# Kernel optimization log

Measured on AMD Instinct MI355X. Metric: run time of the kernel, lower is better.

## Reference

```python
import jax, jax.numpy as jnp
import numpy as np

EMBED = 2048
HEADS = 32
HEAD_DIM = 64
MLP_DIM = 8192
TILE = 16
TOP_K = 12
THETA = 500000.0
EPS = 1e-5
NEG = -1e30


def setup_inputs() -> dict:
    key = jax.random.key(0)
    ks = jax.random.split(key, 9)
    B, S = 2, 1024
    w = lambda k, i, o: jax.random.normal(k, (i, o), jnp.float32) * (i ** -0.5)
    return {
        "x": jax.random.normal(ks[0], (B, S, EMBED), jnp.float32),
        "attn_norm_scale": jnp.ones((EMBED,), jnp.float32),
        "wq": w(ks[1], EMBED, HEADS * HEAD_DIM),
        "wk": w(ks[2], EMBED, HEADS * HEAD_DIM),
        "wv": w(ks[3], EMBED, HEADS * HEAD_DIM),
        "wo": w(ks[4], HEADS * HEAD_DIM, EMBED),
        "ffn_norm_scale": jnp.ones((EMBED,), jnp.float32),
        "w_gate": w(ks[5], EMBED, MLP_DIM),
        "w_up": w(ks[6], EMBED, MLP_DIM),
        "w_down": w(ks[7], MLP_DIM, EMBED),
    }


def _rmsnorm(h, g):
    return h * jax.lax.rsqrt(jnp.mean(h * h, axis=-1, keepdims=True) + EPS) * g


def _rope(t, cos, sin):
    # t: [B,S,H,D]; rotate interleaved pairs (llama precompute_freqs_cis style)
    t1, t2 = t[..., 0::2], t[..., 1::2]
    return jnp.stack([t1 * cos - t2 * sin, t1 * sin + t2 * cos], axis=-1).reshape(t.shape)


def reference(x, attn_norm_scale, wq, wk, wv, wo, ffn_norm_scale, w_gate, w_up, w_down):
    B, S, E = x.shape
    n = _rmsnorm(x, attn_norm_scale)
    q = (n @ wq).reshape(B, S, HEADS, HEAD_DIM)
    k = (n @ wk).reshape(B, S, HEADS, HEAD_DIM)
    v = (n @ wv).reshape(B, S, HEADS, HEAD_DIM)

    inv = 1.0 / (THETA ** (jnp.arange(0, HEAD_DIM, 2, dtype=jnp.float32) / HEAD_DIM))
    ang = jnp.arange(S, dtype=jnp.float32)[:, None] * inv  # [S, D/2]
    cos = jnp.cos(ang)[None, :, None, :]
    sin = jnp.sin(ang)[None, :, None, :]
    q = _rope(q, cos, sin)
    k = _rope(k, cos, sin)

    scale = HEAD_DIM ** -0.5
    scores = jnp.einsum("bqhd,bkhd->bhqk", q, k) * scale  # [B,H,S,S]
    causal = jnp.tril(jnp.ones((S, S), dtype=bool))

    # Kascade anchor: per-query top-k key-tile selection on causally-masked scores
    T = S // TILE
    masked = jnp.where(causal, scores, NEG)
    tile_logits = masked.reshape(B, HEADS, S, T, TILE).max(axis=-1)  # [B,H,S,T]
    _, idx = jax.lax.top_k(tile_logits, TOP_K)  # [B,H,S,K]
    sel = jax.nn.one_hot(idx, T, dtype=jnp.float32).sum(axis=-2) > 0  # [B,H,S,T]
    own = jax.nn.one_hot(jnp.arange(S) // TILE, T, dtype=jnp.float32)[None, None] > 0
    key_mask = jnp.repeat(sel | own, TILE, axis=-1)  # [B,H,S,S]
    allowed = key_mask & causal

    probs = jax.nn.softmax(jnp.where(allowed, scores, NEG), axis=-1)
    attn = jnp.einsum("bhqk,bkhd->bqhd", probs, v).reshape(B, S, HEADS * HEAD_DIM)
    x = x + attn @ wo

    n2 = _rmsnorm(x, ffn_norm_scale)
    mlp = (jax.nn.silu(n2 @ w_gate) * (n2 @ w_up)) @ w_down
    return x + mlp
```

## Files before the change

kernel.cpp:

```cpp
#include <hip/hip_runtime.h>
#include <math.h>

typedef __bf16 bf16_t;
typedef bf16_t bf16x8 __attribute__((ext_vector_type(8)));
typedef bf16_t bf16x2 __attribute__((ext_vector_type(2)));
typedef float f32x4 __attribute__((ext_vector_type(4)));

#define EMBED 2048
#define NHEADS 32
#define HDIM 64
#define MLP 8192
#define SEQ 1024
#define NTOK 2048
#define QKV_N 6144

__device__ __forceinline__ void async_copy16(void* lds, const void* g) {
    __builtin_amdgcn_global_load_lds(
        (const __attribute__((address_space(1))) unsigned int*)g,
        (__attribute__((address_space(3))) unsigned int*)lds, 16, 0, 0);
}

template<int CTRL>
__device__ __forceinline__ float dpp_f(float x) {
    return __int_as_float(__builtin_amdgcn_update_dpp(
        __float_as_int(x), __float_as_int(x), CTRL, 0xF, 0xF, false));
}
__device__ __forceinline__ float rowmax16(float v) {
    v = fmaxf(v, dpp_f<0x121>(v));
    v = fmaxf(v, dpp_f<0x122>(v));
    v = fmaxf(v, dpp_f<0x124>(v));
    v = fmaxf(v, dpp_f<0x128>(v));
    return v;
}
__device__ __forceinline__ float rowsum16(float v) {
    v += dpp_f<0x121>(v);
    v += dpp_f<0x122>(v);
    v += dpp_f<0x124>(v);
    v += dpp_f<0x128>(v);
    return v;
}

template<int EPI>
__global__ __launch_bounds__(256) void gemm_bt(
    const bf16_t* __restrict__ A, const bf16_t* __restrict__ Bt,
    void* __restrict__ Cout, const float* __restrict__ Res,
    const bf16_t* __restrict__ Aux,
    int M, int N, int K)
{
    __shared__ __align__(16) bf16_t As[128 * 32];
    __shared__ __align__(16) bf16_t Bs[128 * 32];
    const int tid = threadIdx.x;
    const int wave = tid >> 6, lane = tid & 63;
    const int quad = lane >> 4, l15 = lane & 15;
    const int wr = wave >> 1, wc = wave & 1;
    const int m0 = blockIdx.x * 128, n0 = blockIdx.y * 128;
    const int srow = lane >> 2;
    const int scol = (lane & 3) * 8;

    f32x4 acc[4][4] = {};

    for (int k0 = 0; k0 < K; k0 += 32) {
        if (k0) __syncthreads();
#pragma unroll
        for (int s = 0; s < 2; ++s) {
            const int chunk = wave * 2 + s;
            const int row = chunk * 16 + srow;
            async_copy16((char*)As + chunk * 1024,
                         A + (size_t)(m0 + row) * K + k0 + scol);
            async_copy16((char*)Bs + chunk * 1024,
                         Bt + (size_t)(n0 + row) * K + k0 + scol);
        }
        asm volatile("s_waitcnt vmcnt(0)" ::: "memory");
        __syncthreads();

        bf16x8 af[4], bfr[4];
#pragma unroll
        for (int i = 0; i < 4; ++i) {
            af[i]  = *(const bf16x8*)((const char*)As + (wr * 64 + i * 16 + l15) * 64 + quad * 16);
            bfr[i] = *(const bf16x8*)((const char*)Bs + (wc * 64 + i * 16 + l15) * 64 + quad * 16);
        }
#pragma unroll
        for (int i = 0; i < 4; ++i)
#pragma unroll
            for (int j = 0; j < 4; ++j)
                acc[i][j] = __builtin_amdgcn_mfma_f32_16x16x32_bf16(af[i], bfr[j], acc[i][j], 0, 0, 0);
    }

#pragma unroll
    for (int i = 0; i < 4; ++i) {
#pragma unroll
        for (int j = 0; j < 4; ++j) {
#pragma unroll
            for (int r = 0; r < 4; ++r) {
                const int row = m0 + wr * 64 + i * 16 + quad * 4 + r;
                const int col = n0 + wc * 64 + j * 16 + l15;
                const size_t idx = (size_t)row * N + col;
                if (EPI == 0) {
                    ((bf16_t*)Cout)[idx] = (bf16_t)acc[i][j][r];
                } else if (EPI == 1) {
                    ((float*)Cout)[idx] = Res[idx] + acc[i][j][r];
                } else {
                    const float g = (float)Aux[idx];
                    const float s = g / (1.0f + __expf(-g));
                    ((bf16_t*)Cout)[idx] = (bf16_t)(s * acc[i][j][r]);
                }
            }
        }
    }
}

__global__ __launch_bounds__(256) void transpose_cvt(
    const float* __restrict__ src, bf16_t* __restrict__ dst, int K, int N)
{
    __shared__ float tile[32][33];
    const int tx = threadIdx.x & 31, ty = threadIdx.x >> 5;
    const int n0 = blockIdx.x * 32, k0 = blockIdx.y * 32;
#pragma unroll
    for (int i = 0; i < 4; ++i)
        tile[ty + 8 * i][tx] = src[(size_t)(k0 + ty + 8 * i) * N + n0 + tx];
    __syncthreads();
#pragma unroll
    for (int i = 0; i < 4; ++i)
        dst[(size_t)(n0 + ty + 8 * i) * K + k0 + tx] = (bf16_t)tile[tx][ty + 8 * i];
}

__global__ __launch_bounds__(256) void rmsnorm_bf16(
    const float* __restrict__ x, const float* __restrict__ g, bf16_t* __restrict__ out)
{
    const int row = blockIdx.x;
    const int tid = threadIdx.x;
    const float* xr = x + (size_t)row * EMBED + tid * 8;
    const float4 a = *(const float4*)xr;
    const float4 b = *(const float4*)(xr + 4);
    float ss = a.x * a.x + a.y * a.y + a.z * a.z + a.w * a.w
             + b.x * b.x + b.y * b.y + b.z * b.z + b.w * b.w;
#pragma unroll
    for (int off = 1; off < 64; off <<= 1) ss += __shfl_xor(ss, off);
    __shared__ float red[4];
    if ((tid & 63) == 0) red[tid >> 6] = ss;
    __syncthreads();
    const float rs = rsqrtf((red[0] + red[1] + red[2] + red[3]) * (1.0f / EMBED) + 1e-5f);
    const float* gr = g + tid * 8;
    const float xv[8] = {a.x, a.y, a.z, a.w, b.x, b.y, b.z, b.w};
    bf16x8 o;
#pragma unroll
    for (int e = 0; e < 8; ++e) o[e] = (bf16_t)(xv[e] * rs * gr[e]);
    *(bf16x8*)(out + (size_t)row * EMBED + tid * 8) = o;
}

__global__ __launch_bounds__(256) void rope_transpose(
    const bf16_t* __restrict__ qkv, bf16_t* __restrict__ Qh, bf16_t* __restrict__ Kh)
{
    const int id = blockIdx.x * 256 + threadIdx.x;
    const int tok = id >> 5;
    const int h = id & 31;
    const int s = tok & (SEQ - 1);
    const int bh = (tok >> 10) * NHEADS + h;
    const size_t dst = ((size_t)bh * SEQ + s) * HDIM;

    const bf16_t* q = qkv + (size_t)tok * QKV_N + h * HDIM;
    const bf16_t* k = q + EMBED;

    const bf16x2* qp = (const bf16x2*)q;
    const bf16x2* kp = (const bf16x2*)k;
    bf16x2* qo = (bf16x2*)(Qh + dst);
    bf16x2* ko = (bf16x2*)(Kh + dst);
    for (int i = 0; i < 32; ++i) {
        const float inv = exp2f((float)i * -0.59161151779f);
        const float ang = (float)s * inv;
        float sn, cs;
        sincosf(ang, &sn, &cs);
        bf16x2 qv = qp[i], kv = kp[i];
        const float q0 = (float)qv[0], q1 = (float)qv[1];
        const float k0 = (float)kv[0], k1 = (float)kv[1];
        qv[0] = (bf16_t)((q0 * cs - q1 * sn) * 0.125f);
        qv[1] = (bf16_t)((q0 * sn + q1 * cs) * 0.125f);
        kv[0] = (bf16_t)(k0 * cs - k1 * sn);
        kv[1] = (bf16_t)(k0 * sn + k1 * cs);
        qo[i] = qv; ko[i] = kv;
    }
}

__global__ __launch_bounds__(256) void transpose_v(
    const bf16_t* __restrict__ qkv, bf16_t* __restrict__ Vt)
{
    __shared__ bf16_t tile[32][66];
    const int st = blockIdx.x;
    const int bh = blockIdx.y;
    const int b = bh >> 5, h = bh & 31;
    const int tid = threadIdx.x;

    const int d = tid & 63, sr = tid >> 6;
    const bf16_t* src = qkv + (size_t)(b * SEQ + st * 32) * QKV_N + 2 * EMBED + h * HDIM;
#pragma unroll
    for (int i = 0; i < 8; ++i) {
        const int s = i * 4 + sr;
        tile[s][d] = src[(size_t)s * QKV_N + d];
    }
    __syncthreads();
    const int s2 = tid & 31, dr = tid >> 5;
    bf16_t* dstp = Vt + (size_t)bh * HDIM * SEQ + st * 32;
#pragma unroll
    for (int i = 0; i < 8; ++i) {
        const int dd = i * 8 + dr;
        dstp[(size_t)dd * SEQ + s2] = tile[s2][dd];
    }
}

__global__ __launch_bounds__(256, 4) void attn_sparse(
    const bf16_t* __restrict__ Qh, const bf16_t* __restrict__ Kh,
    const bf16_t* __restrict__ Vt, bf16_t* __restrict__ attn)
{
    const int qg = blockIdx.x;
    const int h  = blockIdx.y;
    const int b  = blockIdx.z;
    const int tid  = threadIdx.x;
    const int wave = tid >> 6, lane = tid & 63;
    const int quad = lane >> 4, l15 = lane & 15;
    const int qt = wave * 16 + qg;

    __shared__ __align__(16) float  tilemax[4][16][68];
    __shared__ __align__(16) bf16_t Plds[4][16][40];
    __shared__ unsigned long long qmask[4][16];

    const size_t hoff = (size_t)(b * NHEADS + h) * SEQ * HDIM;
    const bf16_t* Qb  = Qh + hoff;
    const bf16_t* Kb  = Kh + hoff;
    const bf16_t* Vtb = Vt + hoff;

    const bf16_t* qrow = Qb + (size_t)(qt * 16 + l15) * HDIM;
    const bf16x8 qf0 = *(const bf16x8*)(qrow + quad * 8);
    const bf16x8 qf1 = *(const bf16x8*)(qrow + 32 + quad * 8);

    const bf16_t* kbase = Kb + (size_t)l15 * HDIM + quad * 8;
    bf16x8 kc0 = *(const bf16x8*)(kbase);
    bf16x8 kc1 = *(const bf16x8*)(kbase + 32);
    for (int t = 0; t <= qt; ++t) {
        const bf16_t* knp = kbase + (size_t)((t < qt) ? t + 1 : t) * (16 * HDIM);
        const bf16x8 kn0 = *(const bf16x8*)(knp);
        const bf16x8 kn1 = *(const bf16x8*)(knp + 32);
        f32x4 sc = {0.f, 0.f, 0.f, 0.f};
        sc = __builtin_amdgcn_mfma_f32_16x16x32_bf16(qf0, kc0, sc, 0, 0, 0);
        sc = __builtin_amdgcn_mfma_f32_16x16x32_bf16(qf1, kc1, sc, 0, 0, 0);
#pragma unroll
        for (int r = 0; r < 4; ++r) {
            const int qr = quad * 4 + r;
            float v = (t == qt && l15 > qr) ? -3.0e38f : sc[r];
            v = rowmax16(v);
            if (l15 == 0) tilemax[wave][qr][t] = v;
        }
        kc0 = kn0; kc1 = kn1;
    }
    asm volatile("s_waitcnt lgkmcnt(0)" ::: "memory");

    if (lane < 16) {
        unsigned long long m = 0;
        const int cnt = qt + 1;
        if (cnt <= 12) {
            m = (1ull << cnt) - 1ull;
        } else {
            const float* tmrow = &tilemax[wave][lane][0];
            const int c4 = qt >> 2;
            for (int it = 0; it < 12; ++it) {
                float best = -3.9e38f; int bi = 0;
                for (int c = 0; c <= c4; ++c) {
                    const float4 v4 = *(const float4*)(tmrow + c * 4);
                    const int tb = c * 4;
                    if (tb + 0 <= qt && !((m >> (tb + 0)) & 1ull) && v4.x > best) { best = v4.x; bi = tb + 0; }
                    if (tb + 1 <= qt && !((m >> (tb + 1)) & 1ull) && v4.y > best) { best = v4.y; bi = tb + 1; }
                    if (tb + 2 <= qt && !((m >> (tb + 2)) & 1ull) && v4.z > best) { best = v4.z; bi = tb + 2; }
                    if (tb + 3 <= qt && !((m >> (tb + 3)) & 1ull) && v4.w > best) { best = v4.w; bi = tb + 3; }
                }
                m |= 1ull << bi;
            }
        }
        m |= 1ull << qt;
        qmask[wave][lane] = m;
    }
    asm volatile("s_waitcnt lgkmcnt(0)" ::: "memory");

    unsigned long long un = 0;
#pragma unroll
    for (int i = 0; i < 16; ++i) un |= qmask[wave][i];
    unsigned long long myrow[4];
#pragma unroll
    for (int r = 0; r < 4; ++r) myrow[r] = qmask[wave][quad * 4 + r];

    float m_run[4], l_run[4];
#pragma unroll
    for (int r = 0; r < 4; ++r) { m_run[r] = -3.0e38f; l_run[r] = 0.f; }
    f32x4 o[4] = {};

    unsigned long long sel = un;
    while (sel) {
        const int t0 = (int)__builtin_ctzll(sel); sel &= sel - 1ull;
        int t1 = -1;
        if (sel) { t1 = (int)__builtin_ctzll(sel); sel &= sel - 1ull; }
        const int t1e = (t1 >= 0) ? t1 : t0;

        const bf16_t* kr0 = Kb + (size_t)(t0 * 16 + l15) * HDIM + quad * 8;
        const bf16x8 k00 = *(const bf16x8*)(kr0);
        const bf16x8 k01 = *(const bf16x8*)(kr0 + 32);
        const bf16_t* kr1 = Kb + (size_t)(t1e * 16 + l15) * HDIM + quad * 8;
        const bf16x8 k10 = *(const bf16x8*)(kr1);
        const bf16x8 k11 = *(const bf16x8*)(kr1 + 32);

        const int colb = ((quad < 2) ? t0 : t1e) * 16 + (quad & 1) * 8;
        bf16x8 vf[4];
#pragma unroll
        for (int jb = 0; jb < 4; ++jb)
            vf[jb] = *(const bf16x8*)(Vtb + (size_t)(jb * 16 + l15) * SEQ + colb);

        f32x4 s0 = {0.f, 0.f, 0.f, 0.f}, s1 = {0.f, 0.f, 0.f, 0.f};
        s0 = __builtin_amdgcn_mfma_f32_16x16x32_bf16(qf0, k00, s0, 0, 0, 0);
        s0 = __builtin_amdgcn_mfma_f32_16x16x32_bf16(qf1, k01, s0, 0, 0, 0);
        s1 = __builtin_amdgcn_mfma_f32_16x16x32_bf16(qf0, k10, s1, 0, 0, 0);
        s1 = __builtin_amdgcn_mfma_f32_16x16x32_bf16(qf1, k11, s1, 0, 0, 0);

#pragma unroll
        for (int r = 0; r < 4; ++r) {
            const int qr = quad * 4 + r;
            const bool ok0 = ((myrow[r] >> t0) & 1ull) && (t0 < qt || l15 <= qr);
            const bool ok1 = (t1 >= 0) && ((myrow[r] >> t1) & 1ull) && (t1 < qt || l15 <= qr);
            const float sv0 = ok0 ? s0[r] : -3.0e38f;
            const float sv1 = ok1 ? s1[r] : -3.0e38f;
            const float mt = rowmax16(fmaxf(sv0, sv1));
            const float mn = fmaxf(m_run[r], mt);
            const float al = __expf(m_run[r] - mn);
            const float p0 = ok0 ? __expf(sv0 - mn) : 0.f;
            const float p1 = ok1 ? __expf(sv1 - mn) : 0.f;
            const float rsum = rowsum16(p0 + p1);
            l_run[r] = l_run[r] * al + rsum;
            m_run[r] = mn;
            Plds[wave][qr][l15]      = (bf16_t)p0;
            Plds[wave][qr][16 + l15] = (bf16_t)p1;
#pragma unroll
            for (int jb = 0; jb < 4; ++jb) o[jb][r] *= al;
        }
        asm volatile("s_waitcnt lgkmcnt(0)" ::: "memory");

        const bf16x8 pa = *(const bf16x8*)&Plds[wave][l15][quad * 8];
#pragma unroll
        for (int jb = 0; jb < 4; ++jb)
            o[jb] = __builtin_amdgcn_mfma_f32_16x16x32_bf16(pa, vf[jb], o[jb], 0, 0, 0);
    }

    const int tok0 = b * SEQ + qt * 16;
#pragma unroll
    for (int r = 0; r < 4; ++r) {
        const int qr = quad * 4 + r;
        const float inv = 1.0f / l_run[r];
        bf16_t* op = attn + (size_t)(tok0 + qr) * EMBED + h * HDIM + l15;
#pragma unroll
        for (int jb = 0; jb < 4; ++jb)
            op[jb * 16] = (bf16_t)(o[jb][r] * inv);
    }
}

extern "C" void kernel_launch(void* const* d_in, const int* in_sizes, int n_in,
                              void* d_out, int out_size, void* d_ws, size_t ws_size,
                              hipStream_t stream)
{
    const float* x   = (const float*)d_in[0];
    const float* ans = (const float*)d_in[1];
    const float* wq  = (const float*)d_in[2];
    const float* wk  = (const float*)d_in[3];
    const float* wv  = (const float*)d_in[4];
    const float* wo  = (const float*)d_in[5];
    const float* fns = (const float*)d_in[6];
    const float* wg  = (const float*)d_in[7];
    const float* wu  = (const float*)d_in[8];
    const float* wd  = (const float*)d_in[9];
    (void)in_sizes; (void)n_in; (void)out_size; (void)ws_size;

    char* ws = (char*)d_ws;
    const size_t MB = 1024 * 1024;
    bf16_t* wt_reg = (bf16_t*)(ws);
    bf16_t* qkv    = (bf16_t*)(ws + 32 * MB);
    bf16_t* attnb  = (bf16_t*)(ws + 56 * MB);
    bf16_t* gate   = (bf16_t*)(ws + 32 * MB);
    float*  x1     = (float* )(ws + 64 * MB);
    bf16_t* nbuf   = (bf16_t*)(ws + 80 * MB);
    bf16_t* Qh     = (bf16_t*)(ws + 88 * MB);
    bf16_t* Kh     = (bf16_t*)(ws + 98 * MB);
    bf16_t* Vt     = (bf16_t*)(ws + 108 * MB);
    bf16_t* hbuf   = (bf16_t*)(ws + 88 * MB);

    transpose_cvt<<<dim3(64, 64), 256, 0, stream>>>(wq, wt_reg,                             EMBED, EMBED);
    transpose_cvt<<<dim3(64, 64), 256, 0, stream>>>(wk, wt_reg + (size_t)EMBED * EMBED,     EMBED, EMBED);
    transpose_cvt<<<dim3(64, 64), 256, 0, stream>>>(wv, wt_reg + (size_t)2 * EMBED * EMBED, EMBED, EMBED);
    rmsnorm_bf16<<<NTOK, 256, 0, stream>>>(x, ans, nbuf);
    gemm_bt<0><<<dim3(16, 48), 256, 0, stream>>>(nbuf, wt_reg, qkv, nullptr, nullptr, NTOK, QKV_N, EMBED);
    rope_transpose<<<256, 256, 0, stream>>>(qkv, Qh, Kh);
    transpose_v<<<dim3(32, 64), 256, 0, stream>>>(qkv, Vt);
    attn_sparse<<<dim3(16, 32, 2), 256, 0, stream>>>(Qh, Kh, Vt, attnb);
    transpose_cvt<<<dim3(64, 64), 256, 0, stream>>>(wo, wt_reg, EMBED, EMBED);
    gemm_bt<1><<<dim3(16, 16), 256, 0, stream>>>(attnb, wt_reg, x1, x, nullptr, NTOK, EMBED, EMBED);

    rmsnorm_bf16<<<NTOK, 256, 0, stream>>>(x1, fns, nbuf);
    transpose_cvt<<<dim3(256, 64), 256, 0, stream>>>(wg, wt_reg, EMBED, MLP);
    gemm_bt<0><<<dim3(16, 64), 256, 0, stream>>>(nbuf, wt_reg, gate, nullptr, nullptr, NTOK, MLP, EMBED);
    transpose_cvt<<<dim3(256, 64), 256, 0, stream>>>(wu, wt_reg, EMBED, MLP);
    gemm_bt<2><<<dim3(16, 64), 256, 0, stream>>>(nbuf, wt_reg, hbuf, nullptr, gate, NTOK, MLP, EMBED);
    transpose_cvt<<<dim3(64, 256), 256, 0, stream>>>(wd, wt_reg, MLP, EMBED);
    gemm_bt<1><<<dim3(16, 16), 256, 0, stream>>>(hbuf, wt_reg, (float*)d_out, x1, nullptr, NTOK, EMBED, MLP);
}
```

Before: 982.7 us.

## Split-K the wo and down-projection GEMMs with atomic accumulation

Adds a split-K mode to the GEMM. The residual is first copied into the output buffer, then partial products from each K-slice are added with float atomics. The o-projection now uses 2 slices and the down-projection uses 4, raising the block count from 256 to 512 and 1024 so more of the GPU's compute units are occupied. The cost is extra copy kernels, atomic traffic, and summation order that is no longer deterministic.

Measured after the change: 957.5 us. 1.03x faster.

```diff
diff --git a/kernel.cpp b/kernel.cpp
--- a/kernel.cpp
+++ b/kernel.cpp
@@ -45,7 +45,7 @@
     const bf16_t* __restrict__ A, const bf16_t* __restrict__ Bt,
     void* __restrict__ Cout, const float* __restrict__ Res,
     const bf16_t* __restrict__ Aux,
-    int M, int N, int K)
+    int M, int N, int K, int LDK)
 {
     __shared__ __align__(16) bf16_t As[128 * 32];
     __shared__ __align__(16) bf16_t Bs[128 * 32];
@@ -54,21 +54,23 @@
     const int quad = lane >> 4, l15 = lane & 15;
     const int wr = wave >> 1, wc = wave & 1;
     const int m0 = blockIdx.x * 128, n0 = blockIdx.y * 128;
+    const int kbeg = blockIdx.z * K;
     const int srow = lane >> 2;
     const int scol = (lane & 3) * 8;
 
     f32x4 acc[4][4] = {};
 
-    for (int k0 = 0; k0 < K; k0 += 32) {
-        if (k0) __syncthreads();
+    for (int kk = 0; kk < K; kk += 32) {
+        const int k0 = kbeg + kk;
+        if (kk) __syncthreads();
 #pragma unroll
         for (int s = 0; s < 2; ++s) {
             const int chunk = wave * 2 + s;
             const int row = chunk * 16 + srow;
             async_copy16((char*)As + chunk * 1024,
-                         A + (size_t)(m0 + row) * K + k0 + scol);
+                         A + (size_t)(m0 + row) * LDK + k0 + scol);
             async_copy16((char*)Bs + chunk * 1024,
-                         Bt + (size_t)(n0 + row) * K + k0 + scol);
+                         Bt + (size_t)(n0 + row) * LDK + k0 + scol);
         }
         asm volatile("s_waitcnt vmcnt(0)" ::: "memory");
         __syncthreads();
@@ -99,14 +101,23 @@
                     ((bf16_t*)Cout)[idx] = (bf16_t)acc[i][j][r];
                 } else if (EPI == 1) {
                     ((float*)Cout)[idx] = Res[idx] + acc[i][j][r];
-                } else {
+                } else if (EPI == 2) {
                     const float g = (float)Aux[idx];
                     const float s = g / (1.0f + __expf(-g));
                     ((bf16_t*)Cout)[idx] = (bf16_t)(s * acc[i][j][r]);
+                } else {
+                    unsafeAtomicAdd(&((float*)Cout)[idx], acc[i][j][r]);
                 }
             }
         }
     }
+}
+
+__global__ __launch_bounds__(256) void copy_f32(
+    const float* __restrict__ src, float* __restrict__ dst)
+{
+    const int i = blockIdx.x * 256 + threadIdx.x;
+    ((float4*)dst)[i] = ((const float4*)src)[i];
 }
 
 __global__ __launch_bounds__(256) void transpose_cvt(
@@ -390,18 +401,20 @@
     transpose_cvt<<<dim3(64, 64), 256, 0, stream>>>(wk, wt_reg + (size_t)EMBED * EMBED,     EMBED, EMBED);
     transpose_cvt<<<dim3(64, 64), 256, 0, stream>>>(wv, wt_reg + (size_t)2 * EMBED * EMBED, EMBED, EMBED);
     rmsnorm_bf16<<<NTOK, 256, 0, stream>>>(x, ans, nbuf);
-    gemm_bt<0><<<dim3(16, 48), 256, 0, stream>>>(nbuf, wt_reg, qkv, nullptr, nullptr, NTOK, QKV_N, EMBED);
+    gemm_bt<0><<<dim3(16, 48), 256, 0, stream>>>(nbuf, wt_reg, qkv, nullptr, nullptr, NTOK, QKV_N, EMBED, EMBED);
     rope_transpose<<<256, 256, 0, stream>>>(qkv, Qh, Kh);
     transpose_v<<<dim3(32, 64), 256, 0, stream>>>(qkv, Vt);
     attn_sparse<<<dim3(16, 32, 2), 256, 0, stream>>>(Qh, Kh, Vt, attnb);
     transpose_cvt<<<dim3(64, 64), 256, 0, stream>>>(wo, wt_reg, EMBED, EMBED);
-    gemm_bt<1><<<dim3(16, 16), 256, 0, stream>>>(attnb, wt_reg, x1, x, nullptr, NTOK, EMBED, EMBED);
+    copy_f32<<<4096, 256, 0, stream>>>(x, x1);
+    gemm_bt<3><<<dim3(16, 16, 2), 256, 0, stream>>>(attnb, wt_reg, x1, nullptr, nullptr, NTOK, EMBED, EMBED / 2, EMBED);
 
     rmsnorm_bf16<<<NTOK, 256, 0, stream>>>(x1, fns, nbuf);
     transpose_cvt<<<dim3(256, 64), 256, 0, stream>>>(wg, wt_reg, EMBED, MLP);
-    gemm_bt<0><<<dim3(16, 64), 256, 0, stream>>>(nbuf, wt_reg, gate, nullptr, nullptr, NTOK, MLP, EMBED);
+    gemm_bt<0><<<dim3(16, 64), 256, 0, stream>>>(nbuf, wt_reg, gate, nullptr, nullptr, NTOK, MLP, EMBED, EMBED);
     transpose_cvt<<<dim3(256, 64), 256, 0, stream>>>(wu, wt_reg, EMBED, MLP);
-    gemm_bt<2><<<dim3(16, 64), 256, 0, stream>>>(nbuf, wt_reg, hbuf, nullptr, gate, NTOK, MLP, EMBED);
+    gemm_bt<2><<<dim3(16, 64), 256, 0, stream>>>(nbuf, wt_reg, hbuf, nullptr, gate, NTOK, MLP, EMBED, EMBED);
     transpose_cvt<<<dim3(64, 256), 256, 0, stream>>>(wd, wt_reg, MLP, EMBED);
-    gemm_bt<1><<<dim3(16, 16), 256, 0, stream>>>(hbuf, wt_reg, (float*)d_out, x1, nullptr, NTOK, EMBED, MLP);
-}
+    copy_f32<<<4096, 256, 0, stream>>>(x1, (float*)d_out);
+    gemm_bt<3><<<dim3(16, 16, 4), 256, 0, stream>>>(hbuf, wt_reg, (float*)d_out, nullptr, nullptr, NTOK, EMBED, MLP / 4, MLP);
+}
```
